# Optimization experiments

Measured on AMD Instinct MI355X. Metric: run time of the kernel, lower is better.

The kernel has to match this reference:

```python
import jax, jax.numpy as jnp
import numpy as np

R = 32
BN_EPS = 1e-5


def _bn(x, g, b):
    # eval-mode BatchNorm with running_mean=0, running_var=1
    shp = (1, -1) + (1,) * (x.ndim - 2)
    scale = g / np.float32(np.sqrt(1.0 + BN_EPS))
    return x * scale.reshape(shp) + b.reshape(shp)


def _conv3d(x, w, b):
    y = jax.lax.conv_general_dilated(x, w, (1, 1, 1), [(1, 1)] * 3,
                                     dimension_numbers=('NCDHW', 'OIDHW', 'NCDHW'))
    return y + b[None, :, None, None, None]


def _conv1d(x, w, b):  # kernel_size=1 conv -> matmul; w [O,I], x [B,I,N]
    return jnp.einsum('oi,bin->bon', w, x) + b[None, :, None]


def _voxelize(features, coords, r):
    # PVCNN Voxelization: detach coords, center, normalize, scatter-average
    coords = jax.lax.stop_gradient(coords)
    c = coords - coords.mean(axis=2, keepdims=True)            # [B,3,N]
    nrm = jnp.linalg.norm(c, axis=1, keepdims=True)            # [B,1,N]
    c = c / (nrm.max(axis=2, keepdims=True) * 2.0) + 0.5
    c = jnp.clip(c * r, 0.0, r - 1.0)                          # float voxel coords
    vox = jnp.round(c).astype(jnp.int32)
    B, C, N = features.shape
    idx = vox[:, 0] * r * r + vox[:, 1] * r + vox[:, 2]        # [B,N]
    flat = (idx + (jnp.arange(B, dtype=jnp.int32) * (r ** 3))[:, None]).reshape(-1)
    feats = features.transpose(0, 2, 1).reshape(B * N, C)
    sums = jax.ops.segment_sum(feats, flat, num_segments=B * r ** 3)
    cnt = jax.ops.segment_sum(jnp.ones((B * N,), features.dtype), flat, num_segments=B * r ** 3)
    grid = sums / jnp.maximum(cnt, 1.0)[:, None]
    grid = grid.reshape(B, r, r, r, C).transpose(0, 4, 1, 2, 3)  # [B,C,r,r,r]
    return grid, c


def _devoxelize(grid, c, r):
    # trilinear interpolation gather at float coords c in [0, r-1]
    B, C = grid.shape[:2]
    lo = jnp.clip(jnp.floor(c).astype(jnp.int32), 0, r - 1)
    hi = jnp.minimum(lo + 1, r - 1)
    f = c - lo.astype(c.dtype)
    gridf = grid.reshape(B, C, r * r * r)
    gather = jax.vmap(lambda g, i: g[:, i])  # per-batch [C,R3],[N] -> [C,N]
    out = jnp.zeros((B, C, c.shape[2]), grid.dtype)
    for ix, wx in ((lo[:, 0], 1.0 - f[:, 0]), (hi[:, 0], f[:, 0])):
        for iy, wy in ((lo[:, 1], 1.0 - f[:, 1]), (hi[:, 1], f[:, 1])):
            for iz, wz in ((lo[:, 2], 1.0 - f[:, 2]), (hi[:, 2], f[:, 2])):
                idx = ix * r * r + iy * r + iz
                out = out + gather(gridf, idx) * (wx * wy * wz)[:, None, :]
    return out


def setup_inputs() -> dict:
    key = jax.random.key(0)
    ks = jax.random.split(key, 24)
    n = lambda k, s, sc=0.05: (jax.random.normal(k, s, dtype=jnp.float32) * sc)
    inp = {
        'features': jax.random.normal(ks[0], (4, 64, 65536), dtype=jnp.float32),
        'coords': jax.random.normal(ks[1], (4, 3, 65536), dtype=jnp.float32),
        'vconv_w': n(ks[2], (64, 64, 3, 3, 3)),
        'vconv_b': n(ks[3], (64,)),
        'vbn_g': 1.0 + n(ks[4], (64,)),
        'vbn_b': n(ks[5], (64,)),
        'res_w': n(ks[6], (2, 2, 64, 64, 3, 3, 3)),
        'res_b': n(ks[7], (2, 2, 64)),
        'res_bn_g': 1.0 + n(ks[8], (2, 2, 64)),
        'res_bn_b': n(ks[9], (2, 2, 64)),
        'pf_w': n(ks[10], (64, 64)),
        'pf_b': n(ks[11], (64,)),
        'pf_bn_g': 1.0 + n(ks[12], (64,)),
        'pf_bn_b': n(ks[13], (64,)),
        'attn_wa': n(ks[14], (16, 64)),
        'attn_ba': n(ks[15], (16,)),
        'attn_wb': n(ks[16], (16, 64)),
        'attn_bb': n(ks[17], (16,)),
        'attn_wc': n(ks[18], (1, 32)),
        'attn_bc': n(ks[19], (1,)),
    }
    return inp


def reference(features, coords, vconv_w, vconv_b, vbn_g, vbn_b,
              res_w, res_b, res_bn_g, res_bn_b,
              pf_w, pf_b, pf_bn_g, pf_bn_b,
              attn_wa, attn_ba, attn_wb, attn_bb, attn_wc, attn_bc):
    grid, nc = _voxelize(features, coords, R)
    # BasicConvolutionBlock
    x = jax.nn.relu(_bn(_conv3d(grid, vconv_w, vconv_b), vbn_g, vbn_b))
    # two ResidualBlocks (inc==outc, stride 1 -> identity downsample)
    for i in range(2):
        y = jax.nn.relu(_bn(_conv3d(x, res_w[i, 0], res_b[i, 0]), res_bn_g[i, 0], res_bn_b[i, 0]))
        y = _bn(_conv3d(y, res_w[i, 1], res_b[i, 1]), res_bn_g[i, 1], res_bn_b[i, 1])
        x = jax.nn.relu(y + x)
    vfeat = _devoxelize(x, nc, R)                               # [B,64,N]
    # SharedMLP: Conv1d(k=1) + BN1d + ReLU
    pfeat = jax.nn.relu(_bn(_conv1d(features, pf_w, pf_b), pf_bn_g, pf_bn_b))
    # Attn fusion (channel dim 64 -> atten_64 branch)
    xa = _conv1d(vfeat, attn_wa, attn_ba)
    xb = _conv1d(pfeat, attn_wb, attn_bb)
    q = _conv1d(jnp.concatenate([xa, xb], axis=1), attn_wc, attn_bc)
    attention = 1.0 + jax.nn.sigmoid(q)
    fused = vfeat * attention + pfeat
    return fused
```

## Files before the change

kernel.cpp:

```cpp
#include <hip/hip_runtime.h>
#include <math.h>

#define NPT 65536
#define NB 4
#define R3 32768

typedef __attribute__((ext_vector_type(8))) short short8;
typedef __attribute__((ext_vector_type(16))) float f32x16;

#define OFF_WB16 0
#define OFF_BEFF 276480
#define OFF_PWB  276800
#define OFF_PB   280896
#define OFF_WAE  280960
#define OFF_WBE  281024
#define OFF_Q0   281088
#define OFF_MEAN 281104
#define OFF_MAXN 281116
#define OFF_PART 281120
#define OFF_AUX  281248
#define OFF_CB3  281504
#define OFF_CUR  1067936
#define OFF_ORD  1199008
#define OFF_GA   1330080
#define OFF_G0   9718688
#define OFF_G1   13912992

__device__ __forceinline__ unsigned short f2b(float f) {
    union { float f; unsigned int u; } v; v.f = f;
    unsigned int r = v.u + 0x7fffu + ((v.u >> 16) & 1u);
    return (unsigned short)(r >> 16);
}
__device__ __forceinline__ float b2f(unsigned short u) {
    union { unsigned int u; float f; } v; v.u = ((unsigned int)u) << 16; return v.f;
}

__global__ void k_setup(const float* __restrict__ vconv_w, const float* __restrict__ vconv_b,
                        const float* __restrict__ vbn_g, const float* __restrict__ vbn_b,
                        const float* __restrict__ res_w, const float* __restrict__ res_b,
                        const float* __restrict__ res_bn_g, const float* __restrict__ res_bn_b,
                        const float* __restrict__ pf_w, const float* __restrict__ pf_b,
                        const float* __restrict__ pf_bn_g, const float* __restrict__ pf_bn_b,
                        const float* __restrict__ wa, const float* __restrict__ ba,
                        const float* __restrict__ wb, const float* __restrict__ bb,
                        const float* __restrict__ wc, const float* __restrict__ bc,
                        float* __restrict__ ws) {
    int idx = blockIdx.x * 256 + threadIdx.x;
    const float invs = rsqrtf(1.00001f);
    if (idx < 552960) {
        unsigned short* wb16 = (unsigned short*)(ws + OFF_WB16);
        int j = idx & 7;
        int l = (idx >> 3) & 63;
        int nh = (idx >> 9) & 1;
        int ks = (idx >> 10) & 3;
        int rest = idx >> 12;
        int t = rest % 27;
        int layer = rest / 27;
        int i = ks * 16 + ((l >> 5) << 3) + j;
        int o = nh * 32 + (l & 31);
        float scale, wsrc;
        if (layer == 0) {
            scale = vbn_g[o] * invs;
            wsrc = vconv_w[(o * 64 + i) * 27 + t];
        } else {
            scale = res_bn_g[(layer - 1) * 64 + o] * invs;
            wsrc = res_w[(size_t)(layer - 1) * 110592 + (o * 64 + i) * 27 + t];
        }
        wb16[idx] = f2b(wsrc * scale);
        return;
    }
    idx -= 552960;
    if (idx < 320) {
        int l = idx >> 6, o = idx & 63;
        float b_, g_, s_;
        if (l == 0) { b_ = vconv_b[o]; g_ = vbn_g[o]; s_ = vbn_b[o]; }
        else {
            b_ = res_b[(l - 1) * 64 + o];
            g_ = res_bn_g[(l - 1) * 64 + o];
            s_ = res_bn_b[(l - 1) * 64 + o];
        }
        ws[OFF_BEFF + idx] = b_ * g_ * invs + s_;
    } else if (idx < 4416) {
        int e = idx - 320;
        int j = e & 7;
        int lane = (e >> 3) & 63;
        int ks = (e >> 9) & 3;
        int half = e >> 11;
        int i = ks * 16 + ((lane >> 5) << 3) + j;
        int o = half * 32 + (lane & 31);
        ((unsigned short*)(ws + OFF_PWB))[e] = f2b(pf_w[o * 64 + i] * pf_bn_g[o] * invs);
    } else if (idx < 4480) {
        int o = idx - 4416;
        ws[OFF_PB + o] = pf_b[o] * pf_bn_g[o] * invs + pf_bn_b[o];
    } else if (idx < 4544) {
        int o = idx - 4480;
        float s = 0.f;
        for (int j = 0; j < 16; j++) s += wc[j] * wa[j * 64 + o];
        ws[OFF_WAE + o] = s;
    } else if (idx < 4608) {
        int o = idx - 4544;
        float s = 0.f;
        for (int j = 0; j < 16; j++) s += wc[16 + j] * wb[j * 64 + o];
        ws[OFF_WBE + o] = s;
    } else if (idx == 4608) {
        float s = bc[0];
        for (int j = 0; j < 16; j++) s += wc[j] * ba[j] + wc[16 + j] * bb[j];
        ws[OFF_Q0] = s;
    }
}

__global__ __launch_bounds__(256) void k_mean1(const float* __restrict__ coords,
                                               float* __restrict__ part,
                                               float4* __restrict__ curz) {
    for (int i = blockIdx.x * 256 + threadIdx.x; i < 32768; i += 96 * 256)
        curz[i] = make_float4(0.f, 0.f, 0.f, 0.f);
    __shared__ float sm[256];
    int bd = blockIdx.x >> 3, chunk = blockIdx.x & 7;
    int tid = threadIdx.x;
    const float* p = coords + (size_t)bd * NPT + chunk * 8192;
    float s = 0.f;
    for (int n = tid; n < 8192; n += 256) s += p[n];
    sm[tid] = s; __syncthreads();
    for (int st = 128; st > 0; st >>= 1) {
        if (tid < st) sm[tid] += sm[tid + st];
        __syncthreads();
    }
    if (tid == 0) part[blockIdx.x] = sm[0];
}

__global__ __launch_bounds__(256) void k_maxn1(const float* __restrict__ coords,
                                               float* __restrict__ part,
                                               float* __restrict__ mean) {
    __shared__ float sm[256];
    int b = blockIdx.x >> 3, chunk = blockIdx.x & 7;
    int tid = threadIdx.x;
    float m0 = 0.f, m1 = 0.f, m2 = 0.f;
    #pragma unroll
    for (int c = 0; c < 8; c++) {
        m0 += part[(b * 3 + 0) * 8 + c];
        m1 += part[(b * 3 + 1) * 8 + c];
        m2 += part[(b * 3 + 2) * 8 + c];
    }
    m0 *= (1.0f / NPT); m1 *= (1.0f / NPT); m2 *= (1.0f / NPT);
    if (chunk == 0 && tid == 0) {
        mean[b * 3] = m0; mean[b * 3 + 1] = m1; mean[b * 3 + 2] = m2;
    }
    const float* p0 = coords + (size_t)(b * 3) * NPT + chunk * 8192;
    float mx = 0.f;
    for (int n = tid; n < 8192; n += 256) {
        float dx = p0[n] - m0, dy = p0[NPT + n] - m1, dz = p0[2 * NPT + n] - m2;
        mx = fmaxf(mx, dx * dx + dy * dy + dz * dz);
    }
    sm[tid] = mx; __syncthreads();
    for (int st = 128; st > 0; st >>= 1) {
        if (tid < st) sm[tid] = fmaxf(sm[tid], sm[tid + st]);
        __syncthreads();
    }
    if (tid == 0) part[96 + blockIdx.x] = sm[0];
}

__global__ void k_prep(const float* __restrict__ coords, const float* __restrict__ mean,
                       const float* __restrict__ part, float* __restrict__ cb3,
                       int* __restrict__ cursor) {
    int gid = blockIdx.x * 256 + threadIdx.x;
    int b = gid >> 16, n = gid & 65535;
    float mx = 0.f;
    #pragma unroll
    for (int c = 0; c < 8; c++) mx = fmaxf(mx, part[96 + b * 8 + c]);
    float inv = 0.5f / sqrtf(mx);
    float c0 = (coords[(size_t)(b * 3) * NPT + n]     - mean[b * 3])     * inv + 0.5f;
    float c1 = (coords[(size_t)(b * 3 + 1) * NPT + n] - mean[b * 3 + 1]) * inv + 0.5f;
    float c2 = (coords[(size_t)(b * 3 + 2) * NPT + n] - mean[b * 3 + 2]) * inv + 0.5f;
    c0 = fminf(fmaxf(c0 * 32.f, 0.f), 31.f);
    c1 = fminf(fmaxf(c1 * 32.f, 0.f), 31.f);
    c2 = fminf(fmaxf(c2 * 32.f, 0.f), 31.f);
    cb3[gid * 3]     = c0;
    cb3[gid * 3 + 1] = c1;
    cb3[gid * 3 + 2] = c2;
    int vx = b * R3 + ((int)rintf(c0) * 1024 + (int)rintf(c1) * 32 + (int)rintf(c2));
    atomicAdd(&cursor[vx], 1);
}

__global__ void k_scan1(int* __restrict__ cur, int* __restrict__ aux) {
    __shared__ int sm[256];
    int t = threadIdx.x;
    int base = blockIdx.x * 512 + t * 2;
    int c0 = cur[base], c1 = cur[base + 1];
    int s = c0 + c1;
    sm[t] = s; __syncthreads();
    for (int off = 1; off < 256; off <<= 1) {
        int v = (t >= off) ? sm[t - off] : 0;
        __syncthreads();
        sm[t] += v;
        __syncthreads();
    }
    int ex = sm[t] - s;
    cur[base] = ex;
    cur[base + 1] = ex + c0;
    if (t == 255) aux[blockIdx.x] = sm[t];
}

__global__ void k_scan3(int* __restrict__ cur, const int* __restrict__ aux) {
    __shared__ int sm[256];
    int t = threadIdx.x;
    sm[t] = (t < blockIdx.x) ? aux[t] : 0;
    __syncthreads();
    for (int off = 128; off > 0; off >>= 1) {
        if (t < off) sm[t] += sm[t + off];
        __syncthreads();
    }
    int add = sm[0];
    int base = blockIdx.x * 512 + t * 2;
    cur[base] += add;
    cur[base + 1] += add;
}

__global__ __launch_bounds__(256) void k_trans(const float* __restrict__ feats,
                                               unsigned short* __restrict__ ft) {
    __shared__ float lds[64][65];
    int b = blockIdx.x >> 10;
    int n0 = (blockIdx.x & 1023) << 6;
    int tid = threadIdx.x;
    int nl = tid & 63;
    #pragma unroll
    for (int it = 0; it < 16; it++) {
        int ch = it * 4 + (tid >> 6);
        lds[nl][ch] = feats[((size_t)(b * 64 + ch) << 16) + n0 + nl];
    }
    __syncthreads();
    int nn = tid >> 2;
    int ch0 = (tid & 3) << 4;
    size_t obase = (((size_t)(b << 16) + n0 + nn) << 6) + ch0;
    short8 v0, v1;
    #pragma unroll
    for (int j = 0; j < 8; j++) v0[j] = (short)f2b(lds[nn][ch0 + j]);
    #pragma unroll
    for (int j = 0; j < 8; j++) v1[j] = (short)f2b(lds[nn][ch0 + 8 + j]);
    *(short8*)(ft + obase) = v0;
    *(short8*)(ft + obase + 8) = v1;
}

__global__ void k_place(const float* __restrict__ cb3, int* __restrict__ cursor,
                        unsigned short* __restrict__ order) {
    int gid = blockIdx.x * 256 + threadIdx.x;
    int b = gid >> 16;
    float c0 = cb3[gid * 3], c1 = cb3[gid * 3 + 1], c2 = cb3[gid * 3 + 2];
    int vx = b * R3 + ((int)rintf(c0) * 1024 + (int)rintf(c1) * 32 + (int)rintf(c2));
    int slot = atomicAdd(&cursor[vx], 1);
    order[slot] = (unsigned short)(gid & 65535);
}

__global__ __launch_bounds__(256) void k_gather(const int* __restrict__ cursor,
        const unsigned short* __restrict__ order, const unsigned short* __restrict__ ft,
        unsigned short* __restrict__ g0) {
    int tid = threadIdx.x;
    int lane = tid & 63;
    int vx = blockIdx.x * 4 + (tid >> 6);
    int e = cursor[vx];
    int s = (vx == 0) ? 0 : cursor[vx - 1];
    int cnt = e - s;
    int p = lane >> 3;
    int g = lane & 7;
    int bb = vx >> 15;
    float acc[8] = {0.f, 0.f, 0.f, 0.f, 0.f, 0.f, 0.f, 0.f};
    for (int base = s; base < e; base += 8) {
        int idx = base + p;
        if (idx < e) {
            int n = order[idx];
            const unsigned short* fp = ft + (((size_t)(bb << 16) + n) << 6) + (g << 3);
            short8 v = *(const short8*)fp;
            #pragma unroll
            for (int j = 0; j < 8; j++) acc[j] += b2f((unsigned short)v[j]);
        }
    }
    #pragma unroll
    for (int j = 0; j < 8; j++) {
        acc[j] += __shfl_xor(acc[j], 8, 64);
        acc[j] += __shfl_xor(acc[j], 16, 64);
        acc[j] += __shfl_xor(acc[j], 32, 64);
    }
    if (p == 0) {
        float inv = 1.0f / (float)max(cnt, 1);
        int col = vx >> 5, z = vx & 31;
        short8 o8;
        #pragma unroll
        for (int j = 0; j < 8; j++) o8[j] = (short)f2b(acc[j] * inv);
        *(short8*)(g0 + (size_t)col * 2048 + (g << 8) + z * 8) = o8;
    }
}

__global__ __launch_bounds__(512) void k_conv(const unsigned short* __restrict__ in,
        const unsigned short* __restrict__ w, const float* __restrict__ bias,
        const float* __restrict__ idF, float* __restrict__ outF,
        unsigned short* __restrict__ out, int zmaj) {
    __shared__ unsigned short sA[18 * 2048];
    int tid = threadIdx.x;
    int lane = tid & 63;
    int wid = tid >> 6;
    int cp = wid & 1;
    int nh = (wid >> 1) & 1;
    int kh = wid >> 2;
    int tile = blockIdx.x;
    int b = blockIdx.y;
    int x = tile >> 3;
    int y0 = (tile & 7) << 2;
    int t = tid & 255;
    int h = tid >> 8;
    int sq = wid & 3;
    #pragma unroll 1
    for (int s2 = 0; s2 < 9; s2++) {
        int s = s2 * 2 + h;
        int gx = x + s / 6 - 1;
        int gy = y0 + s % 6 - 1;
        if ((unsigned)gx < 32u && (unsigned)gy < 32u) {
            const unsigned short* gsrc = in + (((size_t)b * 1024 + gx * 32 + gy) << 11)
                                            + ((size_t)t << 3);
            __builtin_amdgcn_global_load_lds(
                (const __attribute__((address_space(1))) unsigned int*)gsrc,
                (__attribute__((address_space(3))) unsigned int*)(sA + s * 2048 + (sq << 9)),
                16, 0, 0);
        } else {
            ((float4*)(sA + s * 2048))[t] = make_float4(0.f, 0.f, 0.f, 0.f);
        }
    }
    __syncthreads();
    f32x16 accA = {}, accB = {};
    const short8 zero8 = {0, 0, 0, 0, 0, 0, 0, 0};
    int half = lane >> 5;
    int z = lane & 31;
    #pragma unroll
    for (int c9 = 0; c9 < 9; c9++) {
        int dxi = c9 / 3, dyi = c9 % 3;
        int s0 = dxi * 6 + dyi + cp * 2;
        const unsigned short* acol0 = sA + s0 * 2048 + (half << 8) + kh * 1024;
        const unsigned short* wbase = w + (dxi * 9 + dyi * 3) * 4096 + nh * 512
                                        + kh * 2048 + lane * 8;
        #pragma unroll
        for (int dzi = 0; dzi < 3; dzi++) {
            int zz = z + dzi - 1;
            bool zv = (unsigned)zz < 32u;
            int zc = zv ? zz : 0;
            const unsigned short* ac0 = acol0 + zc * 8;
            const unsigned short* wp = wbase + dzi * 4096;
            #pragma unroll
            for (int ksi = 0; ksi < 2; ksi++) {
                short8 bf = *(const short8*)(wp + ksi * 1024);
                short8 a0 = *(const short8*)(ac0 + ksi * 512);
                short8 a1 = *(const short8*)(ac0 + 2048 + ksi * 512);
                if (!zv) { a0 = zero8; a1 = zero8; }
                accA = __builtin_amdgcn_mfma_f32_32x32x16_bf16(a0, bf, accA, 0, 0, 0);
                accB = __builtin_amdgcn_mfma_f32_32x32x16_bf16(a1, bf, accB, 0, 0, 0);
            }
        }
    }
    __syncthreads();
    float* RED = (float*)sA;
    if (kh == 1) {
        #pragma unroll
        for (int c = 0; c < 2; c++) {
            const f32x16& a = c ? accB : accA;
            #pragma unroll
            for (int rb = 0; rb < 4; rb++) {
                float4 v = make_float4(a[rb * 4], a[rb * 4 + 1], a[rb * 4 + 2], a[rb * 4 + 3]);
                ((float4*)(RED + ((((cp * 2 + nh) * 2 + c) * 4 + rb) << 8)))[lane] = v;
            }
        }
    }
    __syncthreads();
    if (kh == 0) {
        #pragma unroll
        for (int rb = 0; rb < 4; rb++) {
            float4 v0 = ((float4*)(RED + ((((cp * 2 + nh) * 2 + 0) * 4 + rb) << 8)))[lane];
            float4 v1 = ((float4*)(RED + ((((cp * 2 + nh) * 2 + 1) * 4 + rb) << 8)))[lane];
            accA[rb * 4]     += v0.x; accA[rb * 4 + 1] += v0.y;
            accA[rb * 4 + 2] += v0.z; accA[rb * 4 + 3] += v0.w;
            accB[rb * 4]     += v1.x; accB[rb * 4 + 1] += v1.y;
            accB[rb * 4 + 2] += v1.z; accB[rb * 4 + 3] += v1.w;
        }
        int o = nh * 32 + (lane & 31);
        float bb = bias[o];
        #pragma unroll
        for (int cc = 0; cc < 2; cc++) {
            int outcol = b * 1024 + x * 32 + (y0 + cp * 2 + cc);
            size_t cbase = (size_t)outcol << 11;
            size_t obase = cbase + (size_t)((o >> 3) << 8) + (o & 7);
            const f32x16& acc = cc ? accB : accA;
            #pragma unroll
            for (int r = 0; r < 16; r++) {
                int zr = (r & 3) + ((r >> 2) << 3) + ((lane >> 5) << 2);
                size_t oe = obase + (size_t)zr * 8;
                float v = acc[r] + bb;
                if (idF) v += idF[oe];
                v = fmaxf(v, 0.f);
                if (zmaj) out[cbase + (size_t)zr * 64 + o] = f2b(v);
                else out[oe] = f2b(v);
                if (outF) outF[oe] = v;
            }
        }
    }
}

__global__ __launch_bounds__(256) void k_pfeat(const float* __restrict__ feats,
        const float* __restrict__ pb, const unsigned short* __restrict__ pwb,
        unsigned short* __restrict__ pf) {
    int tid = threadIdx.x;
    int lane = tid & 63;
    int wv = tid >> 6;
    int tile = blockIdx.x * 4 + wv;
    int b = tile >> 11;
    int n0 = (tile & 2047) << 5;
    int m = lane & 31, kg = lane >> 5;
    const float* fb = feats + ((size_t)b << 22) + n0 + m;
    f32x16 acc0 = {}, acc1 = {};
    #pragma unroll
    for (int ks = 0; ks < 4; ks++) {
        short8 af;
        #pragma unroll
        for (int j = 0; j < 8; j++)
            af[j] = (short)f2b(fb[(size_t)(ks * 16 + kg * 8 + j) << 16]);
        short8 b0 = *(const short8*)(pwb + ((size_t)(ks * 64 + lane) << 3));
        short8 b1 = *(const short8*)(pwb + ((size_t)((4 + ks) * 64 + lane) << 3));
        acc0 = __builtin_amdgcn_mfma_f32_32x32x16_bf16(af, b0, acc0, 0, 0, 0);
        acc1 = __builtin_amdgcn_mfma_f32_32x32x16_bf16(af, b1, acc1, 0, 0, 0);
    }
    int och = lane & 31;
    float bias0 = pb[och], bias1 = pb[32 + och];
    #pragma unroll
    for (int r = 0; r < 16; r++) {
        int p = (r & 3) + ((r >> 2) << 3) + ((lane >> 5) << 2);
        size_t base = ((size_t)(b << 16) + n0 + p) << 6;
        pf[base + och]      = f2b(fmaxf(acc0[r] + bias0, 0.f));
        pf[base + 32 + och] = f2b(fmaxf(acc1[r] + bias1, 0.f));
    }
}

__global__ __launch_bounds__(256) void k_final(const float* __restrict__ cb3,
        const unsigned short* __restrict__ gb, const unsigned short* __restrict__ pfeat,
        const float* __restrict__ ws, float* __restrict__ out) {
    int tid = threadIdx.x;
    int lane = tid & 63;
    int g = lane >> 3;
    int p = lane & 7;
    int b = blockIdx.y;
    int n = (blockIdx.x << 5) + ((tid >> 6) << 3) + p;
    int gid = (b << 16) + n;
    float c0 = cb3[gid * 3], c1 = cb3[gid * 3 + 1], c2 = cb3[gid * 3 + 2];
    int lx = (int)floorf(c0), ly = (int)floorf(c1), lz = (int)floorf(c2);
    int hx = min(lx + 1, 31), hy = min(ly + 1, 31), hz = min(lz + 1, 31);
    float fx = c0 - (float)lx, fy = c1 - (float)ly, fz = c2 - (float)lz;
    int xs[2] = {lx, hx}; float wxx[2] = {1.f - fx, fx};
    int ys[2] = {ly, hy}; float wyy[2] = {1.f - fy, fy};
    int zs[2] = {lz, hz}; float wzz[2] = {1.f - fz, fz};
    float vf[8];
    #pragma unroll
    for (int j = 0; j < 8; j++) vf[j] = 0.f;
    #pragma unroll
    for (int ii = 0; ii < 2; ii++)
    #pragma unroll
    for (int jj = 0; jj < 2; jj++)
    #pragma unroll
    for (int kk = 0; kk < 2; kk++) {
        float wgt = wxx[ii] * wyy[jj] * wzz[kk];
        const unsigned short* gp = gb + (((size_t)b * 1024 + xs[ii] * 32 + ys[jj]) << 11)
                                      + zs[kk] * 64 + (g << 3);
        short8 v = *(const short8*)gp;
        #pragma unroll
        for (int j = 0; j < 8; j++) vf[j] += wgt * b2f((unsigned short)v[j]);
    }
    float pfv[8];
    const unsigned short* pp = pfeat + ((size_t)gid << 6) + (g << 3);
    short8 pv = *(const short8*)pp;
    #pragma unroll
    for (int j = 0; j < 8; j++) pfv[j] = b2f((unsigned short)pv[j]);
    const float* wae = ws + OFF_WAE + (g << 3);
    const float* wbe = ws + OFF_WBE + (g << 3);
    float part = 0.f;
    #pragma unroll
    for (int j = 0; j < 8; j++) part += wae[j] * vf[j] + wbe[j] * pfv[j];
    part += __shfl_xor(part, 8, 64);
    part += __shfl_xor(part, 16, 64);
    part += __shfl_xor(part, 32, 64);
    float q = part + ws[OFF_Q0];
    float attn = 1.0f + 1.0f / (1.0f + expf(-q));
    float* op = out + (((size_t)(b * 64 + (g << 3))) << 16) + n;
    #pragma unroll
    for (int j = 0; j < 8; j++) op[(size_t)j << 16] = vf[j] * attn + pfv[j];
}

extern "C" void kernel_launch(void* const* d_in, const int* in_sizes, int n_in,
                              void* d_out, int out_size, void* d_ws, size_t ws_size,
                              hipStream_t stream) {
    const float* features = (const float*)d_in[0];
    const float* coords   = (const float*)d_in[1];
    const float* vconv_w  = (const float*)d_in[2];
    const float* vconv_b  = (const float*)d_in[3];
    const float* vbn_g    = (const float*)d_in[4];
    const float* vbn_b    = (const float*)d_in[5];
    const float* res_w    = (const float*)d_in[6];
    const float* res_b    = (const float*)d_in[7];
    const float* res_bn_g = (const float*)d_in[8];
    const float* res_bn_b = (const float*)d_in[9];
    const float* pf_w     = (const float*)d_in[10];
    const float* pf_b     = (const float*)d_in[11];
    const float* pf_bn_g  = (const float*)d_in[12];
    const float* pf_bn_b  = (const float*)d_in[13];
    const float* attn_wa  = (const float*)d_in[14];
    const float* attn_ba  = (const float*)d_in[15];
    const float* attn_wb  = (const float*)d_in[16];
    const float* attn_bb  = (const float*)d_in[17];
    const float* attn_wc  = (const float*)d_in[18];
    const float* attn_bc  = (const float*)d_in[19];
    float* ws  = (float*)d_ws;
    float* out = (float*)d_out;

    unsigned short* WB  = (unsigned short*)(ws + OFF_WB16);
    unsigned short* PWB = (unsigned short*)(ws + OFF_PWB);
    int*            CUR = (int*)(ws + OFF_CUR);
    int*            AUX = (int*)(ws + OFF_AUX);
    unsigned short* ORD = (unsigned short*)(ws + OFF_ORD);
    unsigned short* FT  = (unsigned short*)(ws + OFF_GA);
    unsigned short* PF  = (unsigned short*)(ws + OFF_GA);
    float* GA = ws + OFF_GA;
    unsigned short* G0 = (unsigned short*)(ws + OFF_G0);
    unsigned short* G1 = (unsigned short*)(ws + OFF_G1);
    const float* Bv = ws + OFF_BEFF;

    k_setup<<<2179, 256, 0, stream>>>(vconv_w, vconv_b, vbn_g, vbn_b, res_w, res_b,
                                      res_bn_g, res_bn_b, pf_w, pf_b, pf_bn_g, pf_bn_b,
                                      attn_wa, attn_ba, attn_wb, attn_bb, attn_wc, attn_bc, ws);
    k_mean1<<<96, 256, 0, stream>>>(coords, ws + OFF_PART, (float4*)CUR);
    k_maxn1<<<32, 256, 0, stream>>>(coords, ws + OFF_PART, ws + OFF_MEAN);
    k_prep<<<1024, 256, 0, stream>>>(coords, ws + OFF_MEAN, ws + OFF_PART,
                                     ws + OFF_CB3, CUR);
    k_scan1<<<256, 256, 0, stream>>>(CUR, AUX);
    k_scan3<<<256, 256, 0, stream>>>(CUR, AUX);
    k_trans<<<4096, 256, 0, stream>>>(features, FT);
    k_place<<<1024, 256, 0, stream>>>(ws + OFF_CB3, CUR, ORD);
    k_gather<<<32768, 256, 0, stream>>>(CUR, ORD, FT, G0);

    dim3 cg(256, 4);
    k_conv<<<cg, 512, 0, stream>>>(G0, WB + 0 * 110592, Bv + 0,   nullptr, GA,      G1, 0);
    k_conv<<<cg, 512, 0, stream>>>(G1, WB + 1 * 110592, Bv + 64,  nullptr, nullptr, G0, 0);
    k_conv<<<cg, 512, 0, stream>>>(G0, WB + 2 * 110592, Bv + 128, GA,      GA,      G1, 0);
    k_conv<<<cg, 512, 0, stream>>>(G1, WB + 3 * 110592, Bv + 192, nullptr, nullptr, G0, 0);
    k_conv<<<cg, 512, 0, stream>>>(G0, WB + 4 * 110592, Bv + 256, GA,      nullptr, G1, 1);

    k_pfeat<<<2048, 256, 0, stream>>>(features, ws + OFF_PB, PWB, PF);

    dim3 fg(2048, 4);
    k_final<<<fg, 256, 0, stream>>>(ws + OFF_CB3, G1, PF, ws, out);
}
```

Before: 533.7 us.

## Software-pipeline conv MFMA loop with prefetched weights and LDS operands

Flattens the 3D conv inner loops into a single 54-step loop. Weight fragments are prefetched three steps ahead from global memory and activation fragments one step ahead from LDS, with a sched_barrier so the loads overlap the MFMAs. Out-of-range z taps now read a zeroed pad region in LDS instead of being masked with a select. It also raises launch bounds to request two blocks per CU, which adds register pressure from the prefetch buffers and risks spilling.

```diff
diff --git a/kernel.cpp b/kernel.cpp
--- a/kernel.cpp
+++ b/kernel.cpp
@@ -289,11 +289,11 @@
     }
 }
 
-__global__ __launch_bounds__(512) void k_conv(const unsigned short* __restrict__ in,
+__global__ __launch_bounds__(512, 2) void k_conv(const unsigned short* __restrict__ in,
         const unsigned short* __restrict__ w, const float* __restrict__ bias,
         const float* __restrict__ idF, float* __restrict__ outF,
         unsigned short* __restrict__ out, int zmaj) {
-    __shared__ unsigned short sA[18 * 2048];
+    __shared__ unsigned short sA[18 * 2048 + 32];
     int tid = threadIdx.x;
     int lane = tid & 63;
     int wid = tid >> 6;
@@ -307,6 +307,15 @@
     int t = tid & 255;
     int h = tid >> 8;
     int sq = wid & 3;
+
+    if (tid < 4) ((float*)sA)[18432 + tid] = 0.f;
+
+    const unsigned short* wl = w + nh * 512 + kh * 2048 + lane * 8;
+    short8 wbuf[4];
+    #pragma unroll
+    for (int s = 0; s < 3; s++)
+        wbuf[s] = *(const short8*)(wl + (s / 6) * 12288 + ((s % 6) / 2) * 4096 + (s & 1) * 1024);
+
     #pragma unroll 1
     for (int s2 = 0; s2 < 9; s2++) {
         int s = s2 * 2 + h;
@@ -324,35 +333,45 @@
         }
     }
     __syncthreads();
+
     f32x16 accA = {}, accB = {};
-    const short8 zero8 = {0, 0, 0, 0, 0, 0, 0, 0};
     int half = lane >> 5;
     int z = lane & 31;
-    #pragma unroll
-    for (int c9 = 0; c9 < 9; c9++) {
-        int dxi = c9 / 3, dyi = c9 % 3;
-        int s0 = dxi * 6 + dyi + cp * 2;
-        const unsigned short* acol0 = sA + s0 * 2048 + (half << 8) + kh * 1024;
-        const unsigned short* wbase = w + (dxi * 9 + dyi * 3) * 4096 + nh * 512
-                                        + kh * 2048 + lane * 8;
-        #pragma unroll
-        for (int dzi = 0; dzi < 3; dzi++) {
+    int abase = (half << 8) + kh * 1024;
+    short8 a0buf[2], a1buf[2];
+    {
+        int zz = z - 1;
+        bool zv = zz >= 0;
+        int base = (cp * 2) * 2048 + abase;
+        int a0 = zv ? (base + zz * 8) : 36864;
+        int a1 = zv ? (base + 2048 + zz * 8) : 36864;
+        a0buf[0] = *(const short8*)(sA + a0);
+        a1buf[0] = *(const short8*)(sA + a1);
+    }
+    #pragma unroll
+    for (int s = 0; s < 54; s++) {
+        if (s < 53) {
+            int sn = s + 1;
+            int c9 = sn / 6, dzi = (sn % 6) / 2;
             int zz = z + dzi - 1;
             bool zv = (unsigned)zz < 32u;
-            int zc = zv ? zz : 0;
-            const unsigned short* ac0 = acol0 + zc * 8;
-            const unsigned short* wp = wbase + dzi * 4096;
-            #pragma unroll
-            for (int ksi = 0; ksi < 2; ksi++) {
-                short8 bf = *(const short8*)(wp + ksi * 1024);
-                short8 a0 = *(const short8*)(ac0 + ksi * 512);
-                short8 a1 = *(const short8*)(ac0 + 2048 + ksi * 512);
-                if (!zv) { a0 = zero8; a1 = zero8; }
-                accA = __builtin_amdgcn_mfma_f32_32x32x16_bf16(a0, bf, accA, 0, 0, 0);
-                accB = __builtin_amdgcn_mfma_f32_32x32x16_bf16(a1, bf, accB, 0, 0, 0);
-            }
-        }
-    }
+            int s0 = (c9 / 3) * 6 + (c9 % 3) + cp * 2;
+            int base = s0 * 2048 + abase + (sn & 1) * 512;
+            int a0 = zv ? (base + zz * 8) : 36864;
+            int a1 = zv ? (base + 2048 + zz * 8) : 36864;
+            a0buf[sn & 1] = *(const short8*)(sA + a0);
+            a1buf[sn & 1] = *(const short8*)(sA + a1);
+        }
+        if (s < 51) {
+            int sw = s + 3;
+            wbuf[sw & 3] = *(const short8*)(wl + (sw / 6) * 12288
+                                             + ((sw % 6) / 2) * 4096 + (sw & 1) * 1024);
+        }
+        __builtin_amdgcn_sched_barrier(0);
+        accA = __builtin_amdgcn_mfma_f32_32x32x16_bf16(a0buf[s & 1], wbuf[s & 3], accA, 0, 0, 0);
+        accB = __builtin_amdgcn_mfma_f32_32x32x16_bf16(a1buf[s & 1], wbuf[s & 3], accB, 0, 0, 0);
+    }
+
     __syncthreads();
     float* RED = (float*)sA;
     if (kh == 1) {
```

After: 514.6 us. 1.04x faster.
